# Kernel optimization log

Measured on AMD Instinct MI355X. Metric: run time of the kernel, lower is better.

The kernel has to match this reference:

```python
import jax, jax.numpy as jnp
import numpy as np

N, E, C = 50000, 300000, 256  # nodes, edges, hidden size


def setup_inputs() -> dict:
    key = jax.random.key(0)
    ks = jax.random.split(key, 12)
    s = 0.05  # param init scale
    return {
        "x": jax.random.normal(ks[0], (N, C), dtype=jnp.float32),
        "edge_index": jax.random.randint(ks[1], (2, E), 0, N, dtype=jnp.int32),
        # GATConv layer 1 (heads=1): shared lin weight, att_src/att_dst vectors, bias
        "W1": jax.random.normal(ks[2], (C, C), dtype=jnp.float32) * s,
        "a1_src": jax.random.normal(ks[3], (C,), dtype=jnp.float32) * s,
        "a1_dst": jax.random.normal(ks[4], (C,), dtype=jnp.float32) * s,
        "b1": jnp.zeros((C,), dtype=jnp.float32),
        # GATConv layer 2
        "W2": jax.random.normal(ks[5], (C, C), dtype=jnp.float32) * s,
        "a2_src": jax.random.normal(ks[6], (C,), dtype=jnp.float32) * s,
        "a2_dst": jax.random.normal(ks[7], (C,), dtype=jnp.float32) * s,
        "b2": jnp.zeros((C,), dtype=jnp.float32),
        # Final Linear (torch convention: W [out, in], y = x @ W.T + b)
        "Wl": jax.random.normal(ks[8], (C, C), dtype=jnp.float32) * s,
        "bl": jnp.zeros((C,), dtype=jnp.float32),
    }


def _gat_conv(x, src, dst, W, a_src, a_dst, b):
    # PyG GATConv, heads=1, negative_slope=0.2, self-loops already appended.
    h = x @ W                                  # [N, C]
    alpha_src = h @ a_src                      # [N]
    alpha_dst = h @ a_dst                      # [N]
    e = jax.nn.leaky_relu(alpha_src[src] + alpha_dst[dst], 0.2)   # [E']
    # numerically stable softmax over incoming edges of each destination node
    m = jax.ops.segment_max(e, dst, num_segments=N)               # [N]
    ex = jnp.exp(e - m[dst])
    den = jax.ops.segment_sum(ex, dst, num_segments=N)            # [N]
    w = ex / den[dst]                                              # [E']
    out = jax.ops.segment_sum(h[src] * w[:, None], dst, num_segments=N)  # [N, C]
    return out + b


def reference(x, edge_index, W1, a1_src, a1_dst, b1, W2, a2_src, a2_dst, b2, Wl, bl):
    # add_self_loops (done inside each GATConv in PyG; appending once to the
    # input edge list is equivalent since both convs see the same edges)
    loops = jnp.arange(N, dtype=edge_index.dtype)
    ei = jnp.concatenate([edge_index, jnp.stack([loops, loops])], axis=1)
    src, dst = ei[0], ei[1]
    x = jax.nn.relu(_gat_conv(x, src, dst, W1, a1_src, a1_dst, b1))
    x = jax.nn.relu(_gat_conv(x, src, dst, W2, a2_src, a2_dst, b2))
    return x @ Wl.T + bl
```

## Files before the change

kernel.cpp:

```cpp
#include <hip/hip_runtime.h>

#define NN 50000
#define EE 300000
#define ET (EE + NN)
#define CD 256
#define PAD_M 50048
#define NB 196

typedef unsigned short ushortT;
typedef short bf16x8 __attribute__((ext_vector_type(8)));
typedef float f32x4 __attribute__((ext_vector_type(4)));

__device__ __forceinline__ ushortT f2b(float f) {
    unsigned u = __builtin_bit_cast(unsigned, f);
    unsigned r = (u + 0x7FFFu + ((u >> 16) & 1u)) >> 16;
    return (ushortT)r;
}
__device__ __forceinline__ float b2f(ushortT b) {
    return __builtin_bit_cast(float, ((unsigned)b) << 16);
}


__global__ void init_kernel(int* __restrict__ deg, float* __restrict__ as_,
                            float* __restrict__ ad_) {
    int i = blockIdx.x * blockDim.x + threadIdx.x;
    if (i < NN) {
        deg[i] = 1;
        as_[i] = 0.f;
        ad_[i] = 0.f;
    }
}

__global__ void zero_alpha_kernel(float* __restrict__ as_, float* __restrict__ ad_) {
    int i = blockIdx.x * blockDim.x + threadIdx.x;
    if (i < NN) {
        as_[i] = 0.f;
        ad_[i] = 0.f;
    }
}

__global__ void count_deg_kernel(const int* __restrict__ ei, int* __restrict__ deg) {
    int i = blockIdx.x * blockDim.x + threadIdx.x;
    if (i < EE) atomicAdd(&deg[ei[EE + i]], 1);
}

__global__ __launch_bounds__(256) void scan_part(const int* __restrict__ deg,
                                                 int* __restrict__ bsum) {
    int i = blockIdx.x * 256 + threadIdx.x;
    int v = (i < NN) ? deg[i] : 0;
#pragma unroll
    for (int off = 32; off > 0; off >>= 1) v += __shfl_down(v, off);
    __shared__ int w[4];
    if ((threadIdx.x & 63) == 0) w[threadIdx.x >> 6] = v;
    __syncthreads();
    if (threadIdx.x == 0) bsum[blockIdx.x] = w[0] + w[1] + w[2] + w[3];
}

__global__ __launch_bounds__(256) void scan_top(const int* __restrict__ bsum,
                                                int* __restrict__ boffs,
                                                int* __restrict__ row_start) {
    __shared__ int s[256];
    int t = threadIdx.x;
    int v = (t < NB) ? bsum[t] : 0;
    s[t] = v;
    __syncthreads();
    for (int off = 1; off < 256; off <<= 1) {
        int x = s[t];
        int y = (t >= off) ? s[t - off] : 0;
        __syncthreads();
        s[t] = x + y;
        __syncthreads();
    }
    if (t < NB) boffs[t] = s[t] - v;
    if (t == 0) row_start[NN] = ET;
}

__global__ __launch_bounds__(256) void scan_fill(const int* __restrict__ deg,
                                                 const int* __restrict__ boffs,
                                                 int* __restrict__ row_start,
                                                 int* __restrict__ fill_pos) {
    __shared__ int s[256];
    int t = threadIdx.x;
    int i = blockIdx.x * 256 + t;
    int v = (i < NN) ? deg[i] : 0;
    s[t] = v;
    __syncthreads();
    for (int off = 1; off < 256; off <<= 1) {
        int x = s[t];
        int y = (t >= off) ? s[t - off] : 0;
        __syncthreads();
        s[t] = x + y;
        __syncthreads();
    }
    int excl = s[t] - v + boffs[blockIdx.x];
    if (i < NN) {
        row_start[i] = excl;
        fill_pos[i] = excl;
    }
}

__global__ void fill_csr_kernel(const int* __restrict__ ei, int* __restrict__ fill_pos,
                                int* __restrict__ srcs) {
    int i = blockIdx.x * blockDim.x + threadIdx.x;
    if (i < EE) {
        int s = ei[i];
        int d = ei[EE + i];
        int p = atomicAdd(&fill_pos[d], 1);
        srcs[p] = s;
    } else if (i < ET) {
        int n = i - EE;
        int p = atomicAdd(&fill_pos[n], 1);
        srcs[p] = n;
    }
}


__global__ __launch_bounds__(256) void cast_x_kernel(const float* __restrict__ in,
                                                     ushortT* __restrict__ out) {
    int id = blockIdx.x * 256 + threadIdx.x;
    float4 v = *(const float4*)(in + (size_t)id * 4);
    ushort4 o;
    o.x = f2b(v.x);
    o.y = f2b(v.y);
    o.z = f2b(v.z);
    o.w = f2b(v.w);
    *(ushort4*)(out + (size_t)id * 4) = o;
}

__global__ __launch_bounds__(256) void castT_kernel(const float* __restrict__ W,
                                                    ushortT* __restrict__ Bt) {
    __shared__ float t[32][33];
    int bx = blockIdx.x * 32;
    int by = blockIdx.y * 32;
    int x = threadIdx.x & 31, y = threadIdx.x >> 5;
    for (int yy = y; yy < 32; yy += 8) t[yy][x] = W[(size_t)(bx + yy) * CD + by + x];
    __syncthreads();
    for (int yy = y; yy < 32; yy += 8)
        Bt[(size_t)(by + yy) * CD + bx + x] = f2b(t[x][yy]);
}

__global__ __launch_bounds__(256) void cast_w_kernel(const float* __restrict__ W,
                                                     ushortT* __restrict__ Bt) {
    int id = blockIdx.x * 256 + threadIdx.x;
    float4 v = *(const float4*)(W + (size_t)id * 4);
    ushort4 o;
    o.x = f2b(v.x);
    o.y = f2b(v.y);
    o.z = f2b(v.z);
    o.w = f2b(v.w);
    *(ushort4*)(Bt + (size_t)id * 4) = o;
}


template <int OUTF32, int ALPHA>
__global__ __launch_bounds__(256) void gemm_mfma(const ushortT* __restrict__ A,
                                                 const ushortT* __restrict__ Bt,
                                                 const float* __restrict__ bias,
                                                 float* __restrict__ outF,
                                                 ushortT* __restrict__ outB,
                                                 const float* __restrict__ a_src,
                                                 const float* __restrict__ a_dst,
                                                 float* __restrict__ as_g,
                                                 float* __restrict__ ad_g,
                                                 int M) {
    __shared__ ushortT As[128 * 32];
    __shared__ ushortT Bs[128 * 32];
    int tid = threadIdx.x;
    int wave = tid >> 6, lane = tid & 63;
    int wm = (wave >> 1) * 64, wn = (wave & 1) * 64;
    int bm = blockIdx.x * 128, bn = blockIdx.y * 128;
    int l15 = lane & 15, quad = lane >> 4;

    f32x4 acc[4][4] = {};

    for (int k0 = 0; k0 < CD; k0 += 32) {
#pragma unroll
        for (int p = 0; p < 2; ++p) {
            int c = p * 256 + wave * 64 + lane;
            int row = c >> 2, piece = c & 3;
            const ushortT* ga = A + (size_t)(bm + row) * CD + k0 + piece * 8;
            const ushortT* gb = Bt + (size_t)(bn + row) * CD + k0 + piece * 8;
            __builtin_amdgcn_global_load_lds(
                (const __attribute__((address_space(1))) void*)ga,
                (__attribute__((address_space(3))) void*)(As + (size_t)(p * 256 + wave * 64) * 8),
                16, 0, 0);
            __builtin_amdgcn_global_load_lds(
                (const __attribute__((address_space(1))) void*)gb,
                (__attribute__((address_space(3))) void*)(Bs + (size_t)(p * 256 + wave * 64) * 8),
                16, 0, 0);
        }
        __syncthreads();

        bf16x8 a[4], b[4];
#pragma unroll
        for (int i = 0; i < 4; ++i)
            a[i] = *(const bf16x8*)(As + (size_t)(wm + i * 16 + l15) * 32 + quad * 8);
#pragma unroll
        for (int j = 0; j < 4; ++j)
            b[j] = *(const bf16x8*)(Bs + (size_t)(wn + j * 16 + l15) * 32 + quad * 8);
#pragma unroll
        for (int i = 0; i < 4; ++i)
#pragma unroll
            for (int j = 0; j < 4; ++j)
                acc[i][j] = __builtin_amdgcn_mfma_f32_16x16x32_bf16(a[i], b[j], acc[i][j], 0, 0, 0);
        __syncthreads();
    }

#pragma unroll
    for (int i = 0; i < 4; ++i) {
#pragma unroll
        for (int j = 0; j < 4; ++j) {
            int col = bn + wn + j * 16 + l15;
            int row0 = bm + wm + i * 16 + quad * 4;
#pragma unroll
            for (int r = 0; r < 4; ++r) {
                int row = row0 + r;
                if (row < M) {
                    float v = acc[i][j][r];
                    if (OUTF32) {
                        v += bias[col];
                        outF[(size_t)row * CD + col] = v;
                    } else {
                        outB[(size_t)row * CD + col] = f2b(v);
                    }
                }
            }
        }
    }

    if (ALPHA) {
        float avs[4], avd[4];
#pragma unroll
        for (int j = 0; j < 4; ++j) {
            int col = bn + wn + j * 16 + l15;
            avs[j] = a_src[col];
            avd[j] = a_dst[col];
        }
#pragma unroll
        for (int i = 0; i < 4; ++i) {
#pragma unroll
            for (int r = 0; r < 4; ++r) {
                int row = bm + wm + i * 16 + quad * 4 + r;
                float ps = 0.f, pd = 0.f;
#pragma unroll
                for (int j = 0; j < 4; ++j) {
                    float v = acc[i][j][r];
                    ps += v * avs[j];
                    pd += v * avd[j];
                }
#pragma unroll
                for (int off = 1; off < 16; off <<= 1) {
                    ps += __shfl_xor(ps, off);
                    pd += __shfl_xor(pd, off);
                }
                if (l15 == 0 && row < M) {
                    atomicAdd(&as_g[row], ps);
                    atomicAdd(&ad_g[row], pd);
                }
            }
        }
    }
}


__device__ __forceinline__ float lrelu02(float x) { return x > 0.f ? x : 0.2f * x; }

__global__ __launch_bounds__(256) void gat_agg(const ushortT* __restrict__ h,
                                               const float* __restrict__ as_,
                                               const float* __restrict__ ad_,
                                               const int* __restrict__ row_start,
                                               const int* __restrict__ srcs,
                                               const float* __restrict__ bias,
                                               ushortT* __restrict__ out) {
    int node = blockIdx.x * 4 + (threadIdx.x >> 6);
    int lane = threadIdx.x & 63;
    if (node >= NN) return;
    int rs = row_start[node];
    int re = row_start[node + 1];
    int deg = re - rs;
    float adst = ad_[node];

    float a0 = 0.f, a1 = 0.f, a2 = 0.f, a3 = 0.f;

    if (deg <= 64) {
        int s_lane = srcs[rs + ((lane < deg) ? lane : 0)];
        float e = (lane < deg) ? lrelu02(as_[s_lane] + adst) : -1e30f;
        float m = e;
#pragma unroll
        for (int off = 1; off < 64; off <<= 1) m = fmaxf(m, __shfl_xor(m, off));
        float ex = (lane < deg) ? __expf(e - m) : 0.f;
        float den = ex;
#pragma unroll
        for (int off = 1; off < 64; off <<= 1) den += __shfl_xor(den, off);
        float wl = ex / den;

        for (int kk = 0; kk < deg; kk += 8) {
            int s[8];
            float w[8];
#pragma unroll
            for (int t = 0; t < 8; ++t) {
                int idx = kk + t;
                int ii = (idx < deg) ? idx : kk;
                int sv = __shfl(s_lane, ii);
                float wv = __shfl(wl, ii);
                s[t] = sv;
                w[t] = (idx < deg) ? wv : 0.f;
            }
            ushort4 hv[8];
#pragma unroll
            for (int t = 0; t < 8; ++t)
                hv[t] = *(const ushort4*)(h + (size_t)s[t] * CD + lane * 4);
#pragma unroll
            for (int t = 0; t < 8; ++t) {
                a0 += w[t] * b2f(hv[t].x);
                a1 += w[t] * b2f(hv[t].y);
                a2 += w[t] * b2f(hv[t].z);
                a3 += w[t] * b2f(hv[t].w);
            }
        }
    } else {
        float m = -1e30f;
        for (int k = rs + lane; k < re; k += 64) {
            float e = lrelu02(as_[srcs[k]] + adst);
            m = fmaxf(m, e);
        }
#pragma unroll
        for (int off = 1; off < 64; off <<= 1) m = fmaxf(m, __shfl_xor(m, off));
        float den = 0.f;
        for (int k = rs + lane; k < re; k += 64) {
            float e = lrelu02(as_[srcs[k]] + adst);
            den += __expf(e - m);
        }
#pragma unroll
        for (int off = 1; off < 64; off <<= 1) den += __shfl_xor(den, off);
        float inv_den = 1.f / den;
        for (int k = rs; k < re; ++k) {
            int s = srcs[k];
            float e = lrelu02(as_[s] + adst);
            float w = __expf(e - m) * inv_den;
            ushort4 hv = *(const ushort4*)(h + (size_t)s * CD + lane * 4);
            a0 += w * b2f(hv.x);
            a1 += w * b2f(hv.y);
            a2 += w * b2f(hv.z);
            a3 += w * b2f(hv.w);
        }
    }

    float4 b4 = *(const float4*)(bias + lane * 4);
    a0 = fmaxf(a0 + b4.x, 0.f);
    a1 = fmaxf(a1 + b4.y, 0.f);
    a2 = fmaxf(a2 + b4.z, 0.f);
    a3 = fmaxf(a3 + b4.w, 0.f);
    ushort4 o;
    o.x = f2b(a0);
    o.y = f2b(a1);
    o.z = f2b(a2);
    o.w = f2b(a3);
    *(ushort4*)(out + (size_t)node * CD + lane * 4) = o;
}


extern "C" void kernel_launch(void* const* d_in, const int* in_sizes, int n_in,
                              void* d_out, int out_size, void* d_ws, size_t ws_size,
                              hipStream_t stream) {
    const float* x = (const float*)d_in[0];
    const int* ei = (const int*)d_in[1];
    const float* W1 = (const float*)d_in[2];
    const float* a1s = (const float*)d_in[3];
    const float* a1d = (const float*)d_in[4];
    const float* b1 = (const float*)d_in[5];
    const float* W2 = (const float*)d_in[6];
    const float* a2s = (const float*)d_in[7];
    const float* a2d = (const float*)d_in[8];
    const float* b2 = (const float*)d_in[9];
    const float* Wl = (const float*)d_in[10];
    const float* bl = (const float*)d_in[11];
    float* out = (float*)d_out;

    char* w = (char*)d_ws;
    ushortT* B0 = (ushortT*)w; w += (size_t)PAD_M * CD * 2;
    ushortT* B1 = (ushortT*)w; w += (size_t)PAD_M * CD * 2;
    ushortT* B2 = (ushortT*)w; w += (size_t)PAD_M * CD * 2;
    ushortT* W1t = (ushortT*)w; w += (size_t)CD * CD * 2;
    ushortT* W2t = (ushortT*)w; w += (size_t)CD * CD * 2;
    ushortT* Wlt = (ushortT*)w; w += (size_t)CD * CD * 2;
    float* as_ = (float*)w; w += (size_t)NN * 4;
    float* ad_ = (float*)w; w += (size_t)NN * 4;
    int* deg = (int*)w; w += (size_t)NN * 4;
    int* fill_pos = (int*)w; w += (size_t)NN * 4;
    int* srcs = (int*)w; w += (size_t)ET * 4;
    int* bsum = (int*)w; w += 1024;
    int* boffs = (int*)w; w += 1024;
    int* row_start = (int*)w; w += (size_t)(NN + 1) * 4;

    init_kernel<<<(NN + 255) / 256, 256, 0, stream>>>(deg, as_, ad_);
    count_deg_kernel<<<(EE + 255) / 256, 256, 0, stream>>>(ei, deg);
    scan_part<<<NB, 256, 0, stream>>>(deg, bsum);
    scan_top<<<1, 256, 0, stream>>>(bsum, boffs, row_start);
    scan_fill<<<NB, 256, 0, stream>>>(deg, boffs, row_start, fill_pos);
    fill_csr_kernel<<<(ET + 255) / 256, 256, 0, stream>>>(ei, fill_pos, srcs);

    cast_x_kernel<<<(NN * CD / 4) / 256, 256, 0, stream>>>(x, B0);
    castT_kernel<<<dim3(8, 8), 256, 0, stream>>>(W1, W1t);
    castT_kernel<<<dim3(8, 8), 256, 0, stream>>>(W2, W2t);
    cast_w_kernel<<<(CD * CD / 4) / 256, 256, 0, stream>>>(Wl, Wlt);

    dim3 ggrid((PAD_M) / 128, 2);
    int nwave_blocks = (NN + 3) / 4;

    gemm_mfma<0, 1><<<ggrid, 256, 0, stream>>>(B0, W1t, nullptr, nullptr, B1,
                                               a1s, a1d, as_, ad_, NN);
    gat_agg<<<nwave_blocks, 256, 0, stream>>>(B1, as_, ad_, row_start, srcs, b1, B2);

    zero_alpha_kernel<<<(NN + 255) / 256, 256, 0, stream>>>(as_, ad_);
    gemm_mfma<0, 1><<<ggrid, 256, 0, stream>>>(B2, W2t, nullptr, nullptr, B1,
                                               a2s, a2d, as_, ad_, NN);
    gat_agg<<<nwave_blocks, 256, 0, stream>>>(B1, as_, ad_, row_start, srcs, b2, B0);

    gemm_mfma<1, 0><<<ggrid, 256, 0, stream>>>(B0, Wlt, bl, out, nullptr,
                                               nullptr, nullptr, nullptr, nullptr, NN);
}
```

Measured before the change: 320.0 us.

## Fuse prep kernels and keep full weight tile resident in LDS for GEMM

Merges the x/weight cast kernels and the init/zero kernels into a single prep launch, using separate alpha buffers per layer so the mid-pipeline zero kernel goes away. The GEMM now loads the whole 128x256 weight slice into XOR-swizzled LDS once and reads A fragments directly from global memory, removing the per-k-step barriers. The goal is fewer launches and less synchronisation. The cost is 64KB of LDS per block, which lowers occupancy, and uncoalesced direct global A loads. The bf16 output stores also drop the row<M guard and now write into padded rows.

```diff
diff --git a/kernel.cpp b/kernel.cpp
--- a/kernel.cpp
+++ b/kernel.cpp
@@ -20,24 +20,54 @@
     return __builtin_bit_cast(float, ((unsigned)b) << 16);
 }
 
-
-__global__ void init_kernel(int* __restrict__ deg, float* __restrict__ as_,
-                            float* __restrict__ ad_) {
-    int i = blockIdx.x * blockDim.x + threadIdx.x;
-    if (i < NN) {
-        deg[i] = 1;
-        as_[i] = 0.f;
-        ad_[i] = 0.f;
-    }
-}
-
-__global__ void zero_alpha_kernel(float* __restrict__ as_, float* __restrict__ ad_) {
-    int i = blockIdx.x * blockDim.x + threadIdx.x;
-    if (i < NN) {
-        as_[i] = 0.f;
-        ad_[i] = 0.f;
-    }
-}
+#define PREP_X 12500
+#define PREP_W1 12564
+#define PREP_W2 12628
+#define PREP_WL 12692
+#define PREP_END 12888
+
+__global__ __launch_bounds__(256) void prep_kernel(
+    const float* __restrict__ x, const float* __restrict__ W1,
+    const float* __restrict__ W2, const float* __restrict__ Wl,
+    ushortT* __restrict__ B0, ushortT* __restrict__ W1t,
+    ushortT* __restrict__ W2t, ushortT* __restrict__ Wlt,
+    int* __restrict__ deg, float* __restrict__ asA, float* __restrict__ adA,
+    float* __restrict__ asB, float* __restrict__ adB) {
+    __shared__ float t[32][33];
+    int b = blockIdx.x, tidx = threadIdx.x;
+    if (b < PREP_X) {
+        int id = b * 256 + tidx;
+        float4 v = *(const float4*)(x + (size_t)id * 4);
+        ushort4 o;
+        o.x = f2b(v.x); o.y = f2b(v.y); o.z = f2b(v.z); o.w = f2b(v.w);
+        *(ushort4*)(B0 + (size_t)id * 4) = o;
+    } else if (b < PREP_W2) {
+        const float* W = (b < PREP_W1) ? W1 : W2;
+        ushortT* Bt = (b < PREP_W1) ? W1t : W2t;
+        int rel = b - ((b < PREP_W1) ? PREP_X : PREP_W1);
+        int bx = (rel & 7) * 32;
+        int by = (rel >> 3) * 32;
+        int xx = tidx & 31, yy = tidx >> 5;
+        for (int y = yy; y < 32; y += 8) t[y][xx] = W[(size_t)(bx + y) * CD + by + xx];
+        __syncthreads();
+        for (int y = yy; y < 32; y += 8)
+            Bt[(size_t)(by + y) * CD + bx + xx] = f2b(t[xx][y]);
+    } else if (b < PREP_WL) {
+        int id = (b - PREP_W2) * 256 + tidx;
+        float4 v = *(const float4*)(Wl + (size_t)id * 4);
+        ushort4 o;
+        o.x = f2b(v.x); o.y = f2b(v.y); o.z = f2b(v.z); o.w = f2b(v.w);
+        *(ushort4*)(Wlt + (size_t)id * 4) = o;
+    } else {
+        int i = (b - PREP_WL) * 256 + tidx;
+        if (i < NN) {
+            deg[i] = 1;
+            asA[i] = 0.f; adA[i] = 0.f;
+            asB[i] = 0.f; adB[i] = 0.f;
+        }
+    }
+}
+
 
 __global__ void count_deg_kernel(const int* __restrict__ ei, int* __restrict__ deg) {
     int i = blockIdx.x * blockDim.x + threadIdx.x;
@@ -115,43 +145,6 @@
 }
 
 
-__global__ __launch_bounds__(256) void cast_x_kernel(const float* __restrict__ in,
-                                                     ushortT* __restrict__ out) {
-    int id = blockIdx.x * 256 + threadIdx.x;
-    float4 v = *(const float4*)(in + (size_t)id * 4);
-    ushort4 o;
-    o.x = f2b(v.x);
-    o.y = f2b(v.y);
-    o.z = f2b(v.z);
-    o.w = f2b(v.w);
-    *(ushort4*)(out + (size_t)id * 4) = o;
-}
-
-__global__ __launch_bounds__(256) void castT_kernel(const float* __restrict__ W,
-                                                    ushortT* __restrict__ Bt) {
-    __shared__ float t[32][33];
-    int bx = blockIdx.x * 32;
-    int by = blockIdx.y * 32;
-    int x = threadIdx.x & 31, y = threadIdx.x >> 5;
-    for (int yy = y; yy < 32; yy += 8) t[yy][x] = W[(size_t)(bx + yy) * CD + by + x];
-    __syncthreads();
-    for (int yy = y; yy < 32; yy += 8)
-        Bt[(size_t)(by + yy) * CD + bx + x] = f2b(t[x][yy]);
-}
-
-__global__ __launch_bounds__(256) void cast_w_kernel(const float* __restrict__ W,
-                                                     ushortT* __restrict__ Bt) {
-    int id = blockIdx.x * 256 + threadIdx.x;
-    float4 v = *(const float4*)(W + (size_t)id * 4);
-    ushort4 o;
-    o.x = f2b(v.x);
-    o.y = f2b(v.y);
-    o.z = f2b(v.z);
-    o.w = f2b(v.w);
-    *(ushort4*)(Bt + (size_t)id * 4) = o;
-}
-
-
 template <int OUTF32, int ALPHA>
 __global__ __launch_bounds__(256) void gemm_mfma(const ushortT* __restrict__ A,
                                                  const ushortT* __restrict__ Bt,
@@ -163,47 +156,46 @@
                                                  float* __restrict__ as_g,
                                                  float* __restrict__ ad_g,
                                                  int M) {
-    __shared__ ushortT As[128 * 32];
-    __shared__ ushortT Bs[128 * 32];
+    __shared__ ushortT Bs[128 * 256];
     int tid = threadIdx.x;
     int wave = tid >> 6, lane = tid & 63;
     int wm = (wave >> 1) * 64, wn = (wave & 1) * 64;
     int bm = blockIdx.x * 128, bn = blockIdx.y * 128;
     int l15 = lane & 15, quad = lane >> 4;
 
+#pragma unroll
+    for (int p = 0; p < 16; ++p) {
+        int c = p * 256 + wave * 64 + lane;
+        int row = c >> 5;
+        int piece = c & 31;
+        int spiece = piece ^ (row & 31);
+        const ushortT* gb = Bt + (size_t)(bn + row) * CD + spiece * 8;
+        __builtin_amdgcn_global_load_lds(
+            (const __attribute__((address_space(1))) void*)gb,
+            (__attribute__((address_space(3))) void*)(Bs + (size_t)(p * 256 + wave * 64) * 8),
+            16, 0, 0);
+    }
+    __syncthreads();
+
     f32x4 acc[4][4] = {};
 
-    for (int k0 = 0; k0 < CD; k0 += 32) {
-#pragma unroll
-        for (int p = 0; p < 2; ++p) {
-            int c = p * 256 + wave * 64 + lane;
-            int row = c >> 2, piece = c & 3;
-            const ushortT* ga = A + (size_t)(bm + row) * CD + k0 + piece * 8;
-            const ushortT* gb = Bt + (size_t)(bn + row) * CD + k0 + piece * 8;
-            __builtin_amdgcn_global_load_lds(
-                (const __attribute__((address_space(1))) void*)ga,
-                (__attribute__((address_space(3))) void*)(As + (size_t)(p * 256 + wave * 64) * 8),
-                16, 0, 0);
-            __builtin_amdgcn_global_load_lds(
-                (const __attribute__((address_space(1))) void*)gb,
-                (__attribute__((address_space(3))) void*)(Bs + (size_t)(p * 256 + wave * 64) * 8),
-                16, 0, 0);
-        }
-        __syncthreads();
-
+#pragma unroll
+    for (int kk = 0; kk < 8; ++kk) {
         bf16x8 a[4], b[4];
 #pragma unroll
         for (int i = 0; i < 4; ++i)
-            a[i] = *(const bf16x8*)(As + (size_t)(wm + i * 16 + l15) * 32 + quad * 8);
-#pragma unroll
-        for (int j = 0; j < 4; ++j)
-            b[j] = *(const bf16x8*)(Bs + (size_t)(wn + j * 16 + l15) * 32 + quad * 8);
+            a[i] = *(const bf16x8*)(A + (size_t)(bm + wm + i * 16 + l15) * CD + kk * 32 + quad * 8);
+        int kc = kk * 4 + quad;
+#pragma unroll
+        for (int j = 0; j < 4; ++j) {
+            int n_local = wn + j * 16 + l15;
+            b[j] = *(const bf16x8*)(Bs + (size_t)n_local * 256 + (size_t)(kc ^ (n_local & 31)) * 8);
+        }
 #pragma unroll
         for (int i = 0; i < 4; ++i)
 #pragma unroll
             for (int j = 0; j < 4; ++j)
                 acc[i][j] = __builtin_amdgcn_mfma_f32_16x16x32_bf16(a[i], b[j], acc[i][j], 0, 0, 0);
-        __syncthreads();
     }
 
 #pragma unroll
@@ -215,14 +207,11 @@
 #pragma unroll
             for (int r = 0; r < 4; ++r) {
                 int row = row0 + r;
-                if (row < M) {
-                    float v = acc[i][j][r];
-                    if (OUTF32) {
-                        v += bias[col];
-                        outF[(size_t)row * CD + col] = v;
-                    } else {
-                        outB[(size_t)row * CD + col] = f2b(v);
-                    }
+                float v = acc[i][j][r];
+                if (OUTF32) {
+                    if (row < M) outF[(size_t)row * CD + col] = v + bias[col];
+                } else {
+                    outB[(size_t)row * CD + col] = f2b(v);
                 }
             }
         }
@@ -384,8 +373,10 @@
     ushortT* W1t = (ushortT*)w; w += (size_t)CD * CD * 2;
     ushortT* W2t = (ushortT*)w; w += (size_t)CD * CD * 2;
     ushortT* Wlt = (ushortT*)w; w += (size_t)CD * CD * 2;
-    float* as_ = (float*)w; w += (size_t)NN * 4;
-    float* ad_ = (float*)w; w += (size_t)NN * 4;
+    float* asA = (float*)w; w += (size_t)NN * 4;
+    float* adA = (float*)w; w += (size_t)NN * 4;
+    float* asB = (float*)w; w += (size_t)NN * 4;
+    float* adB = (float*)w; w += (size_t)NN * 4;
     int* deg = (int*)w; w += (size_t)NN * 4;
     int* fill_pos = (int*)w; w += (size_t)NN * 4;
     int* srcs = (int*)w; w += (size_t)ET * 4;
@@ -393,29 +384,25 @@
     int* boffs = (int*)w; w += 1024;
     int* row_start = (int*)w; w += (size_t)(NN + 1) * 4;
 
-    init_kernel<<<(NN + 255) / 256, 256, 0, stream>>>(deg, as_, ad_);
+    prep_kernel<<<PREP_END, 256, 0, stream>>>(x, W1, W2, Wl, B0, W1t, W2t, Wlt,
+                                              deg, asA, adA, asB, adB);
+
     count_deg_kernel<<<(EE + 255) / 256, 256, 0, stream>>>(ei, deg);
     scan_part<<<NB, 256, 0, stream>>>(deg, bsum);
     scan_top<<<1, 256, 0, stream>>>(bsum, boffs, row_start);
     scan_fill<<<NB, 256, 0, stream>>>(deg, boffs, row_start, fill_pos);
     fill_csr_kernel<<<(ET + 255) / 256, 256, 0, stream>>>(ei, fill_pos, srcs);
 
-    cast_x_kernel<<<(NN * CD / 4) / 256, 256, 0, stream>>>(x, B0);
-    castT_kernel<<<dim3(8, 8), 256, 0, stream>>>(W1, W1t);
-    castT_kernel<<<dim3(8, 8), 256, 0, stream>>>(W2, W2t);
-    cast_w_kernel<<<(CD * CD / 4) / 256, 256, 0, stream>>>(Wl, Wlt);
-
     dim3 ggrid((PAD_M) / 128, 2);
     int nwave_blocks = (NN + 3) / 4;
 
     gemm_mfma<0, 1><<<ggrid, 256, 0, stream>>>(B0, W1t, nullptr, nullptr, B1,
-                                               a1s, a1d, as_, ad_, NN);
-    gat_agg<<<nwave_blocks, 256, 0, stream>>>(B1, as_, ad_, row_start, srcs, b1, B2);
-
-    zero_alpha_kernel<<<(NN + 255) / 256, 256, 0, stream>>>(as_, ad_);
+                                               a1s, a1d, asA, adA, NN);
+    gat_agg<<<nwave_blocks, 256, 0, stream>>>(B1, asA, adA, row_start, srcs, b1, B2);
+
     gemm_mfma<0, 1><<<ggrid, 256, 0, stream>>>(B2, W2t, nullptr, nullptr, B1,
-                                               a2s, a2d, as_, ad_, NN);
-    gat_agg<<<nwave_blocks, 256, 0, stream>>>(B1, as_, ad_, row_start, srcs, b2, B0);
+                                               a2s, a2d, asB, adB, NN);
+    gat_agg<<<nwave_blocks, 256, 0, stream>>>(B1, asB, adB, row_start, srcs, b2, B0);
 
     gemm_mfma<1, 0><<<ggrid, 256, 0, stream>>>(B0, Wlt, bl, out, nullptr,
                                                nullptr, nullptr, nullptr, nullptr, NN);
```

After: 319.5 us. No clear change (-0.2%).
